# Kernel optimization log

Hardware: AMD Instinct MI355X
Metric: run time of the kernel (lower is better)

The kernel has to match this reference:

```python
import jax, jax.numpy as jnp
import numpy as np

B, N, DIN, DOUT = 8192, 4, 1024, 256

def setup_inputs() -> dict:
    key = jax.random.key(0)
    k1, k2, k3, k4 = jax.random.split(key, 4)
    adj = jax.random.uniform(k1, (N, N), dtype=jnp.float32)
    features = jax.random.normal(k2, (B, N, DIN), dtype=jnp.float32)
    # nn.Linear(input_size, output_size): weight [DOUT, DIN], bias [DOUT]
    bound = 1.0 / np.sqrt(DIN)
    W = jax.random.uniform(k3, (DOUT, DIN), dtype=jnp.float32, minval=-bound, maxval=bound)
    b = jax.random.uniform(k4, (DOUT,), dtype=jnp.float32, minval=-bound, maxval=bound)
    return {"adj": adj, "features": features, "W": W, "b": b}

def reference(adj, features, W, b):
    # Batched equivalent of: for i in B: linear(adj @ features[i]) -> [B, 4, DOUT]
    h = jnp.einsum("nm,bmf->bnf", adj, features)  # [B, N, DIN]
    return jnp.einsum("bnf,of->bno", h, W) + b    # [B, N, DOUT]
```

## Files before the change

kernel.cpp:

```cpp
#include <hip/hip_runtime.h>


#define DIN 1024
#define DOUT 256
#define BM 64
#define KI 16
#define LDB 72
#define A_HALFS (BM * LDB)

typedef __bf16 bf16x8 __attribute__((ext_vector_type(8)));
typedef float f32x4 __attribute__((ext_vector_type(4)));
typedef unsigned short u16x8 __attribute__((ext_vector_type(8)));

__device__ __forceinline__ unsigned short f2bf(float f) {
  union { float f; unsigned int u; } v;
  v.f = f;
  unsigned int u = v.u;
  u += 0x7fffu + ((u >> 16) & 1u);
  return (unsigned short)(u >> 16);
}

__global__ __launch_bounds__(256) void wprep_kernel(
    const float* __restrict__ W, unsigned short* __restrict__ ws) {
  const int t = blockIdx.x * 256 + threadIdx.x;
  const f32x4* src = (const f32x4*)(W + (size_t)t * 8);
  f32x4 a = src[0], b = src[1];
  u16x8 pk;
#pragma unroll
  for (int m = 0; m < 4; ++m) {
    pk[m] = f2bf(a[m]);
    pk[4 + m] = f2bf(b[m]);
  }
  *(u16x8*)(ws + (size_t)t * 8) = pk;
}

__global__ __launch_bounds__(256, 3) void gconv_kernel(
    const float* __restrict__ adj, const float* __restrict__ feat,
    const unsigned short* __restrict__ wbf, const float* __restrict__ bias,
    float* __restrict__ out) {
  __shared__ __align__(16) unsigned short sA[2][A_HALFS];

  const int tid = threadIdx.x;
  const int bM = blockIdx.x * BM;

  const int row0 = tid >> 3;
  const int kc0 = (tid & 7) * 8;
  const float* aptr0 = feat + (size_t)(bM + row0) * DIN + kc0;
  const float* aptr1 = aptr0 + (size_t)32 * DIN;
  unsigned short* sw0 = &sA[0][row0 * LDB + kc0];
  unsigned short* sw1 = &sA[1][row0 * LDB + kc0];

  const int lane = tid & 63;
  const int wid = tid >> 6;
  const int wc = wid * 64;
  const int rl = lane & 15;
  const int q = lane >> 4;
  const int q8 = q * 8;

  const unsigned short* bp0 = wbf + (size_t)(wc + rl) * DIN + q8;

  f32x4 acc[4][4];
#pragma unroll
  for (int i = 0; i < 4; ++i)
#pragma unroll
    for (int j = 0; j < 4; ++j) acc[i][j] = f32x4{0.f, 0.f, 0.f, 0.f};

  f32x4 pa0 = *(const f32x4*)aptr0;
  f32x4 pa1 = *(const f32x4*)(aptr0 + 4);
  f32x4 pa2 = *(const f32x4*)aptr1;
  f32x4 pa3 = *(const f32x4*)(aptr1 + 4);
  {
    u16x8 pk0, pk1;
#pragma unroll
    for (int m = 0; m < 4; ++m) {
      pk0[m] = f2bf(pa0[m]);
      pk0[4 + m] = f2bf(pa1[m]);
      pk1[m] = f2bf(pa2[m]);
      pk1[4 + m] = f2bf(pa3[m]);
    }
    *(u16x8*)sw0 = pk0;
    *(u16x8*)(sw0 + 32 * LDB) = pk1;
  }
  pa0 = *(const f32x4*)(aptr0 + 64);
  pa1 = *(const f32x4*)(aptr0 + 68);
  pa2 = *(const f32x4*)(aptr1 + 64);
  pa3 = *(const f32x4*)(aptr1 + 68);

  for (int kb = 0; kb < KI; ++kb) {
    bf16x8 bfr[2][4];
#pragma unroll
    for (int ks = 0; ks < 2; ++ks)
#pragma unroll
      for (int j = 0; j < 4; ++j)
        bfr[ks][j] =
            *(const bf16x8*)(bp0 + (size_t)j * 16 * DIN + kb * 64 + ks * 32);

    __builtin_amdgcn_sched_barrier(0);
    asm volatile("s_waitcnt lgkmcnt(0)" ::: "memory");
    __builtin_amdgcn_s_barrier();
    __builtin_amdgcn_sched_barrier(0);

    const unsigned short* sa = (kb & 1) ? &sA[1][0] : &sA[0][0];
#pragma unroll
    for (int ks = 0; ks < 2; ++ks) {
      const int ko = ks * 32 + q8;
      bf16x8 af[4];
#pragma unroll
      for (int i = 0; i < 4; ++i)
        af[i] = *(const bf16x8*)(sa + (i * 16 + rl) * LDB + ko);
#pragma unroll
      for (int i = 0; i < 4; ++i)
#pragma unroll
        for (int j = 0; j < 4; ++j)
          acc[i][j] = __builtin_amdgcn_mfma_f32_16x16x32_bf16(
              af[i], bfr[ks][j], acc[i][j], 0, 0, 0);
    }

    if (kb + 1 < KI) {
      u16x8 pk0, pk1;
#pragma unroll
      for (int m = 0; m < 4; ++m) {
        pk0[m] = f2bf(pa0[m]);
        pk0[4 + m] = f2bf(pa1[m]);
        pk1[m] = f2bf(pa2[m]);
        pk1[4 + m] = f2bf(pa3[m]);
      }
      unsigned short* sw = ((kb + 1) & 1) ? sw1 : sw0;
      *(u16x8*)sw = pk0;
      *(u16x8*)(sw + 32 * LDB) = pk1;
      if (kb + 2 < KI) {
        const float* a0 = aptr0 + (size_t)(kb + 2) * 64;
        const float* a1 = aptr1 + (size_t)(kb + 2) * 64;
        pa0 = *(const f32x4*)a0;
        pa1 = *(const f32x4*)(a0 + 4);
        pa2 = *(const f32x4*)a1;
        pa3 = *(const f32x4*)(a1 + 4);
      }
    }
  }

  float am[16];
#pragma unroll
  for (int i = 0; i < 16; ++i) am[i] = adj[i];

  float bv[4];
#pragma unroll
  for (int j = 0; j < 4; ++j) bv[j] = bias[wc + j * 16 + rl];

#pragma unroll
  for (int i = 0; i < 4; ++i) {
    const size_t rowbase = (size_t)(bM + i * 16 + q * 4);
#pragma unroll
    for (int j = 0; j < 4; ++j) {
      const int col = wc + j * 16 + rl;
      float* op = out + rowbase * DOUT + col;
      f32x4 g = acc[i][j];
#pragma unroll
      for (int n = 0; n < 4; ++n) {
        op[(size_t)n * DOUT] = am[n * 4 + 0] * g[0] + am[n * 4 + 1] * g[1] +
                               am[n * 4 + 2] * g[2] + am[n * 4 + 3] * g[3] +
                               bv[j];
      }
    }
  }
}

extern "C" void kernel_launch(void* const* d_in, const int* in_sizes, int n_in,
                              void* d_out, int out_size, void* d_ws,
                              size_t ws_size, hipStream_t stream) {
  const float* adj = (const float*)d_in[0];
  const float* feat = (const float*)d_in[1];
  const float* W = (const float*)d_in[2];
  const float* bias = (const float*)d_in[3];
  float* out = (float*)d_out;
  unsigned short* ws = (unsigned short*)d_ws;

  wprep_kernel<<<128, 256, 0, stream>>>(W, ws);
  gconv_kernel<<<8192 * 4 / BM, 256, 0, stream>>>(adj, feat, ws, bias, out);
}
```

Before: 222.4 us.

## Drop LDS staging and W prep kernel; load fp32 operands directly into registers

Removes the separate W-to-bf16 prep kernel and the shared-memory double buffer for features. Each wave now loads fp32 feature and W fragments straight from global memory into registers and converts them to bf16 there before the MFMAs. Barriers and one launch go away, and occupancy is lowered to 2 blocks per SM. In exchange, all four waves of a block redundantly load and convert the same feature rows. W is also re-read as fp32, doubling its bytes, and every block converts it again.

```diff
diff --git a/kernel.cpp b/kernel.cpp
--- a/kernel.cpp
+++ b/kernel.cpp
@@ -5,8 +5,6 @@
 #define DOUT 256
 #define BM 64
 #define KI 16
-#define LDB 72
-#define A_HALFS (BM * LDB)
 
 typedef __bf16 bf16x8 __attribute__((ext_vector_type(8)));
 typedef float f32x4 __attribute__((ext_vector_type(4)));
@@ -20,35 +18,22 @@
   return (unsigned short)(u >> 16);
 }
 
-__global__ __launch_bounds__(256) void wprep_kernel(
-    const float* __restrict__ W, unsigned short* __restrict__ ws) {
-  const int t = blockIdx.x * 256 + threadIdx.x;
-  const f32x4* src = (const f32x4*)(W + (size_t)t * 8);
-  f32x4 a = src[0], b = src[1];
-  u16x8 pk;
+__device__ __forceinline__ bf16x8 pack8(f32x4 lo, f32x4 hi) {
+  union { u16x8 u; bf16x8 b; } r;
 #pragma unroll
   for (int m = 0; m < 4; ++m) {
-    pk[m] = f2bf(a[m]);
-    pk[4 + m] = f2bf(b[m]);
+    r.u[m] = f2bf(lo[m]);
+    r.u[4 + m] = f2bf(hi[m]);
   }
-  *(u16x8*)(ws + (size_t)t * 8) = pk;
+  return r.b;
 }
 
-__global__ __launch_bounds__(256, 3) void gconv_kernel(
+__global__ __launch_bounds__(256, 2) void gconv_kernel(
     const float* __restrict__ adj, const float* __restrict__ feat,
-    const unsigned short* __restrict__ wbf, const float* __restrict__ bias,
+    const float* __restrict__ W, const float* __restrict__ bias,
     float* __restrict__ out) {
-  __shared__ __align__(16) unsigned short sA[2][A_HALFS];
-
   const int tid = threadIdx.x;
   const int bM = blockIdx.x * BM;
-
-  const int row0 = tid >> 3;
-  const int kc0 = (tid & 7) * 8;
-  const float* aptr0 = feat + (size_t)(bM + row0) * DIN + kc0;
-  const float* aptr1 = aptr0 + (size_t)32 * DIN;
-  unsigned short* sw0 = &sA[0][row0 * LDB + kc0];
-  unsigned short* sw1 = &sA[1][row0 * LDB + kc0];
 
   const int lane = tid & 63;
   const int wid = tid >> 6;
@@ -57,7 +42,8 @@
   const int q = lane >> 4;
   const int q8 = q * 8;
 
-  const unsigned short* bp0 = wbf + (size_t)(wc + rl) * DIN + q8;
+  const float* ab = feat + (size_t)(bM + rl) * DIN + q8;
+  const float* bb = W + (size_t)(wc + rl) * DIN + q8;
 
   f32x4 acc[4][4];
 #pragma unroll
@@ -65,78 +51,60 @@
 #pragma unroll
     for (int j = 0; j < 4; ++j) acc[i][j] = f32x4{0.f, 0.f, 0.f, 0.f};
 
-  f32x4 pa0 = *(const f32x4*)aptr0;
-  f32x4 pa1 = *(const f32x4*)(aptr0 + 4);
-  f32x4 pa2 = *(const f32x4*)aptr1;
-  f32x4 pa3 = *(const f32x4*)(aptr1 + 4);
-  {
-    u16x8 pk0, pk1;
+  f32x4 a4[4][2][2];
 #pragma unroll
-    for (int m = 0; m < 4; ++m) {
-      pk0[m] = f2bf(pa0[m]);
-      pk0[4 + m] = f2bf(pa1[m]);
-      pk1[m] = f2bf(pa2[m]);
-      pk1[4 + m] = f2bf(pa3[m]);
-    }
-    *(u16x8*)sw0 = pk0;
-    *(u16x8*)(sw0 + 32 * LDB) = pk1;
-  }
-  pa0 = *(const f32x4*)(aptr0 + 64);
-  pa1 = *(const f32x4*)(aptr0 + 68);
-  pa2 = *(const f32x4*)(aptr1 + 64);
-  pa3 = *(const f32x4*)(aptr1 + 68);
+  for (int i = 0; i < 4; ++i)
+#pragma unroll
+    for (int ks = 0; ks < 2; ++ks)
+#pragma unroll
+      for (int h = 0; h < 2; ++h)
+        a4[i][ks][h] =
+            *(const f32x4*)(ab + (size_t)i * 16 * DIN + ks * 32 + h * 4);
 
   for (int kb = 0; kb < KI; ++kb) {
+    f32x4 b4[4][2][2];
+#pragma unroll
+    for (int j = 0; j < 4; ++j)
+#pragma unroll
+      for (int ks = 0; ks < 2; ++ks)
+#pragma unroll
+        for (int h = 0; h < 2; ++h)
+          b4[j][ks][h] = *(const f32x4*)(bb + (size_t)j * 16 * DIN + kb * 64 +
+                                         ks * 32 + h * 4);
+
+    bf16x8 af[2][4];
+#pragma unroll
+    for (int ks = 0; ks < 2; ++ks)
+#pragma unroll
+      for (int i = 0; i < 4; ++i)
+        af[ks][i] = pack8(a4[i][ks][0], a4[i][ks][1]);
+
+    if (kb + 1 < KI) {
+#pragma unroll
+      for (int i = 0; i < 4; ++i)
+#pragma unroll
+        for (int ks = 0; ks < 2; ++ks)
+#pragma unroll
+          for (int h = 0; h < 2; ++h)
+            a4[i][ks][h] = *(const f32x4*)(ab + (size_t)i * 16 * DIN +
+                                           (kb + 1) * 64 + ks * 32 + h * 4);
+    }
+
     bf16x8 bfr[2][4];
 #pragma unroll
     for (int ks = 0; ks < 2; ++ks)
 #pragma unroll
       for (int j = 0; j < 4; ++j)
-        bfr[ks][j] =
-            *(const bf16x8*)(bp0 + (size_t)j * 16 * DIN + kb * 64 + ks * 32);
+        bfr[ks][j] = pack8(b4[j][ks][0], b4[j][ks][1]);
 
-    __builtin_amdgcn_sched_barrier(0);
-    asm volatile("s_waitcnt lgkmcnt(0)" ::: "memory");
-    __builtin_amdgcn_s_barrier();
-    __builtin_amdgcn_sched_barrier(0);
-
-    const unsigned short* sa = (kb & 1) ? &sA[1][0] : &sA[0][0];
 #pragma unroll
-    for (int ks = 0; ks < 2; ++ks) {
-      const int ko = ks * 32 + q8;
-      bf16x8 af[4];
-#pragma unroll
-      for (int i = 0; i < 4; ++i)
-        af[i] = *(const bf16x8*)(sa + (i * 16 + rl) * LDB + ko);
+    for (int ks = 0; ks < 2; ++ks)
 #pragma unroll
       for (int i = 0; i < 4; ++i)
 #pragma unroll
         for (int j = 0; j < 4; ++j)
           acc[i][j] = __builtin_amdgcn_mfma_f32_16x16x32_bf16(
-              af[i], bfr[ks][j], acc[i][j], 0, 0, 0);
-    }
-
-    if (kb + 1 < KI) {
-      u16x8 pk0, pk1;
-#pragma unroll
-      for (int m = 0; m < 4; ++m) {
-        pk0[m] = f2bf(pa0[m]);
-        pk0[4 + m] = f2bf(pa1[m]);
-        pk1[m] = f2bf(pa2[m]);
-        pk1[4 + m] = f2bf(pa3[m]);
-      }
-      unsigned short* sw = ((kb + 1) & 1) ? sw1 : sw0;
-      *(u16x8*)sw = pk0;
-      *(u16x8*)(sw + 32 * LDB) = pk1;
-      if (kb + 2 < KI) {
-        const float* a0 = aptr0 + (size_t)(kb + 2) * 64;
-        const float* a1 = aptr1 + (size_t)(kb + 2) * 64;
-        pa0 = *(const f32x4*)a0;
-        pa1 = *(const f32x4*)(a0 + 4);
-        pa2 = *(const f32x4*)a1;
-        pa3 = *(const f32x4*)(a1 + 4);
-      }
-    }
+              af[ks][i], bfr[ks][j], acc[i][j], 0, 0, 0);
   }
 
   float am[16];
@@ -173,8 +141,8 @@
   const float* W = (const float*)d_in[2];
   const float* bias = (const float*)d_in[3];
   float* out = (float*)d_out;
-  unsigned short* ws = (unsigned short*)d_ws;
+  (void)d_ws;
+  (void)ws_size;
 
-  wprep_kernel<<<128, 256, 0, stream>>>(W, ws);
-  gconv_kernel<<<8192 * 4 / BM, 256, 0, stream>>>(adj, feat, ws, bias, out);
+  gconv_kernel<<<8192 * 4 / BM, 256, 0, stream>>>(adj, feat, W, bias, out);
 }
```

Result: slower. 278.4 us (+25.2%).
